# Optimization experiments

Measured on AMD Instinct MI355X. Metric: run time of the kernel, lower is better.

Reference implementation:

```python
import jax, jax.numpy as jnp
import numpy as np
import math

D_MODEL, N_HEADS, D_HEAD = 1024, 16, 64
INIT_RANGE = 0.02
IGNORE = -100000.0


def setup_inputs() -> dict:
    key = jax.random.key(0)
    ks = jax.random.split(key, 5)
    x = jax.random.normal(ks[0], (2, 2048, D_MODEL), dtype=jnp.float32)
    W_Q = INIT_RANGE * jax.random.normal(ks[1], (N_HEADS, D_MODEL, D_HEAD), dtype=jnp.float32)
    W_K = INIT_RANGE * jax.random.normal(ks[2], (N_HEADS, D_MODEL, D_HEAD), dtype=jnp.float32)
    W_V = INIT_RANGE * jax.random.normal(ks[3], (N_HEADS, D_MODEL, D_HEAD), dtype=jnp.float32)
    # W_O is contracted as 'n_heads d_head d_model' in the original einsum
    W_O = INIT_RANGE * jax.random.normal(ks[4], (N_HEADS, D_HEAD, D_MODEL), dtype=jnp.float32)
    b_Q = jnp.zeros((N_HEADS, D_HEAD), dtype=jnp.float32)
    b_K = jnp.zeros((N_HEADS, D_HEAD), dtype=jnp.float32)
    b_V = jnp.zeros((N_HEADS, D_HEAD), dtype=jnp.float32)
    b_O = jnp.zeros((D_MODEL,), dtype=jnp.float32)
    return {"normalized_resid_pre": x, "W_Q": W_Q, "b_Q": b_Q, "W_K": W_K, "b_K": b_K,
            "W_V": W_V, "b_V": b_V, "W_O": W_O, "b_O": b_O}


def reference(normalized_resid_pre, W_Q, b_Q, W_K, b_K, W_V, b_V, W_O, b_O):
    x = normalized_resid_pre  # [b, s, d_model]
    q = jnp.einsum('bsd,hde->bshe', x, W_Q) + b_Q  # [b, s, h, d_head]
    k = jnp.einsum('bsd,hde->bshe', x, W_K) + b_K
    v = jnp.einsum('bsd,hde->bshe', x, W_V) + b_V
    scores = jnp.einsum('bqhe,bkhe->bhqk', q, k) / math.sqrt(D_HEAD)
    S = x.shape[1]
    causal = jnp.tril(jnp.ones((S, S), dtype=bool))  # True where allowed
    scores = jnp.where(causal, scores, IGNORE)
    pattern = jax.nn.softmax(scores, axis=-1)  # [b, h, q, k]
    z = jnp.einsum('bhqk,bkhe->bqhe', pattern, v)
    attn_out = jnp.einsum('bqhe,hed->bqd', z, W_O) + b_O
    return attn_out
```

## Files before the change

### kernel.cpp

```cpp
#include <hip/hip_runtime.h>
#include <cstdint>
#include <cstddef>

typedef unsigned short u16;
typedef __bf16 bf16x8 __attribute__((ext_vector_type(8)));
typedef _Float16 f16x4 __attribute__((ext_vector_type(4)));
typedef _Float16 f16x2 __attribute__((ext_vector_type(2)));
typedef float  f32x4  __attribute__((ext_vector_type(4)));
typedef unsigned short u16x8 __attribute__((ext_vector_type(8)));
typedef unsigned short u16x4 __attribute__((ext_vector_type(4)));

#define DM   1024
#define NH   16
#define DH   64
#define SS   2048
#define BSZ  4096
#define NQKV 3072
#define QSCALE 0.18033688011f

__device__ __forceinline__ u16 f2b(float f) {
  unsigned u = __builtin_bit_cast(unsigned, f);
  return (u16)((u + 0x7FFFu + ((u >> 16) & 1u)) >> 16);
}
__device__ __forceinline__ u16 f2h(float f) {
  _Float16 h = (_Float16)f;
  return __builtin_bit_cast(u16, h);
}

__device__ __forceinline__ void gl_lds16(const void* g, void* l) {
  __builtin_amdgcn_global_load_lds(
      (__attribute__((address_space(1))) void*)(void*)g,
      (__attribute__((address_space(3))) void*)l, 16, 0, 0);
}

__global__ __launch_bounds__(256) void prep_all_kernel(
    const float* __restrict__ x, u16* __restrict__ xb,
    const float* __restrict__ Wq, const float* __restrict__ Wk,
    const float* __restrict__ Wv, u16* __restrict__ wqkvt,
    const float* __restrict__ Wo, u16* __restrict__ wot) {
  __shared__ __align__(16) u16 Ts[64 * 72];
  int bid = blockIdx.x, t = threadIdx.x;
  if (bid < 2048) {
    int i = (bid * 256 + t) * 8;
    float4 a = *(const float4*)(x + i);
    float4 b = *(const float4*)(x + i + 4);
    u16x8 o;
    o[0] = f2b(a.x); o[1] = f2b(a.y); o[2] = f2b(a.z); o[3] = f2b(a.w);
    o[4] = f2b(b.x); o[5] = f2b(b.y); o[6] = f2b(b.z); o[7] = f2b(b.w);
    *(u16x8*)(xb + i) = o;
    return;
  }
  if (bid < 2816) {
    int idx = bid - 2048;
    int dt = idx & 15, sl = idx >> 4;
    int proj = sl >> 4, h = sl & 15;
    const float* W = (proj == 0) ? Wq : ((proj == 1) ? Wk : Wv);
    int d0 = dt * 64;
    {
      int ld = t >> 2;
      int ec = (t & 3) * 16;
      const float* src = W + ((size_t)h * DM + d0 + ld) * DH + ec;
      float4 v0 = *(const float4*)(src);
      float4 v1 = *(const float4*)(src + 4);
      float4 v2 = *(const float4*)(src + 8);
      float4 v3 = *(const float4*)(src + 12);
      float vv[16] = {v0.x, v0.y, v0.z, v0.w, v1.x, v1.y, v1.z, v1.w,
                      v2.x, v2.y, v2.z, v2.w, v3.x, v3.y, v3.z, v3.w};
#pragma unroll
      for (int i = 0; i < 16; i++) Ts[(ec + i) * 72 + ld] = f2b(vv[i]);
    }
    __syncthreads();
    {
      int le = t >> 2;
      int dc = (t & 3) * 16;
      int n = proj * DM + h * DH + le;
      u16* dst = wqkvt + (size_t)n * DM + d0 + dc;
      *(u16x8*)(dst)     = *(const u16x8*)&Ts[le * 72 + dc];
      *(u16x8*)(dst + 8) = *(const u16x8*)&Ts[le * 72 + dc + 8];
    }
    return;
  }
  {
    int idx = bid - 2816;
    int dt = idx & 15, h = idx >> 4;
    int d0 = dt * 64;
    {
      int le = t >> 2;
      int dc = (t & 3) * 16;
      const float* src = Wo + ((size_t)h * DH + le) * DM + d0 + dc;
      float4 v0 = *(const float4*)(src);
      float4 v1 = *(const float4*)(src + 4);
      float4 v2 = *(const float4*)(src + 8);
      float4 v3 = *(const float4*)(src + 12);
      float vv[16] = {v0.x, v0.y, v0.z, v0.w, v1.x, v1.y, v1.z, v1.w,
                      v2.x, v2.y, v2.z, v2.w, v3.x, v3.y, v3.z, v3.w};
#pragma unroll
      for (int i = 0; i < 16; i++) Ts[(dc + i) * 72 + le] = f2b(vv[i]);
    }
    __syncthreads();
    {
      int ld = t >> 2;
      int ec = (t & 3) * 16;
      u16* dst = wot + (size_t)(d0 + ld) * DM + h * DH + ec;
      *(u16x8*)(dst)     = *(const u16x8*)&Ts[ld * 72 + ec];
      *(u16x8*)(dst + 8) = *(const u16x8*)&Ts[ld * 72 + ec + 8];
    }
  }
}

__global__ __launch_bounds__(256) void gemm_qkv_kernel(
    const u16* __restrict__ A, const u16* __restrict__ Bt,
    u16* __restrict__ o_q, u16* __restrict__ o_k, u16* __restrict__ o_v,
    const float* __restrict__ c0, const float* __restrict__ c1,
    const float* __restrict__ c2) {
  const int K = DM;
  __shared__ __align__(16) u16 As[128 * 32];
  __shared__ __align__(16) u16 Bs[128 * 32];
  __shared__ __align__(16) u16 Cs[64 * 128];
  int t = threadIdx.x, w = t >> 6, l = t & 63;
  int lr = l & 15, lq = l >> 4;
  int m0 = blockIdx.x * 128, n0 = blockIdx.y * 128;
  int wr = w >> 1, wc = w & 1;
  f32x4 acc[4][4] = {};
  const u16* ga = A + (size_t)(m0 + (t >> 2)) * K + (t & 3) * 8;
  const u16* gb = Bt + (size_t)(n0 + (t >> 2)) * K + (t & 3) * 8;

  for (int k0 = 0; k0 < K; k0 += 32) {
    __syncthreads();
    gl_lds16(ga + k0,           &As[w * 512]);
    gl_lds16(ga + k0 + 64 * K,  &As[2048 + w * 512]);
    gl_lds16(gb + k0,           &Bs[w * 512]);
    gl_lds16(gb + k0 + 64 * K,  &Bs[2048 + w * 512]);
    __syncthreads();
    bf16x8 af[4], bfr[4];
#pragma unroll
    for (int i = 0; i < 4; i++)
      af[i] = *(const bf16x8*)&As[(wr * 64 + i * 16 + lr) * 32 + lq * 8];
#pragma unroll
    for (int j = 0; j < 4; j++)
      bfr[j] = *(const bf16x8*)&Bs[(wc * 64 + j * 16 + lr) * 32 + lq * 8];
#pragma unroll
    for (int i = 0; i < 4; i++)
#pragma unroll
      for (int j = 0; j < 4; j++)
        acc[i][j] = __builtin_amdgcn_mfma_f32_16x16x32_bf16(af[i], bfr[j], acc[i][j], 0, 0, 0);
  }

  int proj = n0 >> 10;
  int r0 = n0 & 1023;
  int h0 = r0 >> 6;
  const float* bp = (proj == 0) ? c0 : ((proj == 1) ? c1 : c2);

#pragma unroll
  for (int p = 0; p < 2; p++) {
    __syncthreads();
    if (wr == p) {
#pragma unroll
      for (int j = 0; j < 4; j++) {
        int nl = wc * 64 + j * 16 + lr;
        float bias = bp[r0 + nl];
#pragma unroll
        for (int i = 0; i < 4; i++) {
#pragma unroll
          for (int g = 0; g < 4; g++) {
            int ml = i * 16 + lq * 4 + g;
            float val = acc[i][j][g] + bias;
            if (proj == 0)      Cs[ml * 128 + nl] = f2b(val * QSCALE);
            else if (proj == 1) Cs[ml * 128 + nl] = f2b(val);
            else                Cs[nl * 64 + ml] = f2h(val);
          }
        }
      }
    }
    __syncthreads();
    int m_base = m0 + p * 64;
    if (proj < 2) {
      int ml = t >> 2, q4 = t & 3;
      int hh = q4 >> 1, e0 = (q4 & 1) * 32;
      int m = m_base + ml, b = m >> 11, s = m & 2047;
      int h = h0 + hh;
      u16* dst = (proj == 0 ? o_q : o_k) + ((size_t)(b * NH + h) * SS + s) * DH + e0;
      const u16* src = &Cs[ml * 128 + hh * 64 + e0];
      *(u16x8*)(dst)      = *(const u16x8*)(src);
      *(u16x8*)(dst + 8)  = *(const u16x8*)(src + 8);
      *(u16x8*)(dst + 16) = *(const u16x8*)(src + 16);
      *(u16x8*)(dst + 24) = *(const u16x8*)(src + 24);
    } else {
      int er = t >> 1, sh = t & 1;
      int hh = er >> 6, e = er & 63;
      int h = h0 + hh;
      int ms = m_base + sh * 32, b = ms >> 11, s = ms & 2047;
      u16* dst = o_v + ((size_t)(b * NH + h) * DH + e) * SS + s;
      const u16* src = &Cs[er * 64 + sh * 32];
      *(u16x8*)(dst)      = *(const u16x8*)(src);
      *(u16x8*)(dst + 8)  = *(const u16x8*)(src + 8);
      *(u16x8*)(dst + 16) = *(const u16x8*)(src + 16);
      *(u16x8*)(dst + 24) = *(const u16x8*)(src + 24);
    }
  }
}

__global__ __launch_bounds__(256) void gemm_o_kernel(
    const u16* __restrict__ A, const u16* __restrict__ Bt,
    const float* __restrict__ bo, float* __restrict__ fout) {
  const int K = DM;
  __shared__ __align__(16) u16 As[128 * 32];
  __shared__ __align__(16) u16 Bs[64 * 32];
  int t = threadIdx.x, w = t >> 6, l = t & 63;
  int lr = l & 15, lq = l >> 4;
  int m0 = blockIdx.x * 128, n0 = blockIdx.y * 64;
  f32x4 acc[2][4] = {};
  const u16* ga = A + (size_t)(m0 + (t >> 2)) * K + (t & 3) * 8;
  const u16* gb = Bt + (size_t)(n0 + (t >> 2)) * K + (t & 3) * 8;

  for (int k0 = 0; k0 < K; k0 += 32) {
    __syncthreads();
    gl_lds16(ga + k0,           &As[w * 512]);
    gl_lds16(ga + k0 + 64 * K,  &As[2048 + w * 512]);
    gl_lds16(gb + k0, &Bs[w * 512]);
    __syncthreads();
    bf16x8 af[2], bfr[4];
#pragma unroll
    for (int i = 0; i < 2; i++)
      af[i] = *(const bf16x8*)&As[(w * 32 + i * 16 + lr) * 32 + lq * 8];
#pragma unroll
    for (int j = 0; j < 4; j++)
      bfr[j] = *(const bf16x8*)&Bs[(j * 16 + lr) * 32 + lq * 8];
#pragma unroll
    for (int i = 0; i < 2; i++)
#pragma unroll
      for (int j = 0; j < 4; j++)
        acc[i][j] = __builtin_amdgcn_mfma_f32_16x16x32_bf16(af[i], bfr[j], acc[i][j], 0, 0, 0);
  }

  int mb = m0 + w * 32 + lq * 4;
  int nb = n0 + lr;
#pragma unroll
  for (int j = 0; j < 4; j++) {
    int n = nb + j * 16;
    float bias = bo[n];
#pragma unroll
    for (int i = 0; i < 2; i++) {
#pragma unroll
      for (int g = 0; g < 4; g++) {
        int m = mb + i * 16 + g;
        fout[(size_t)m * DM + n] = acc[i][j][g] + bias;
      }
    }
  }
}

__global__ __launch_bounds__(256) void attn_kernel(const u16* __restrict__ q_ws,
                                                   const u16* __restrict__ k_ws,
                                                   const u16* __restrict__ vt_ws,
                                                   u16* __restrict__ z_ws) {
  __shared__ __align__(16) u16 Ks[2][64 * 72], Vs[2][64 * 72];

  int t = threadIdx.x;
  int w = t >> 6;
  int l = t & 63;
  int lr = l & 15, lq = l >> 4;
  int srow = t >> 3;
  int sc8 = (t & 7) * 8;

  int bid = blockIdx.x;
  int xcd = bid & 7, idx = bid >> 3;
  int bh = xcd * 4 + (idx & 3);
  int p = idx >> 2;
  int bq = p & 7;
  int jt = (p >> 3) ? (15 - bq) : bq;
  const u16* Qb = q_ws + (size_t)bh * SS * DH;
  const u16* Kb = k_ws + (size_t)bh * SS * DH;
  const u16* Vb = vt_ws + (size_t)bh * DH * SS;
  int b = bh >> 4, h16 = bh & 15;

  int q0 = jt * 128;
  int nkt = 2 * jt + 2;
  int my_last = nkt - 2 + (w >> 1);

  int qr0 = q0 + w * 32 + lr;
  bf16x8 qf00 = *(const bf16x8*)(Qb + (size_t)qr0 * DH + lq * 8);
  bf16x8 qf01 = *(const bf16x8*)(Qb + (size_t)qr0 * DH + 32 + lq * 8);
  bf16x8 qf10 = *(const bf16x8*)(Qb + (size_t)(qr0 + 16) * DH + lq * 8);
  bf16x8 qf11 = *(const bf16x8*)(Qb + (size_t)(qr0 + 16) * DH + 32 + lq * 8);

  f32x4 accO0[4] = {}, accO1[4] = {};
  float accL0 = 0.f, accL1 = 0.f;

  {
    const u16* kg = Kb + (size_t)srow * DH + sc8;
    const u16* vg = Vb + (size_t)srow * SS + sc8;
    *(u16x8*)&Ks[0][srow * 72 + sc8] = *(const u16x8*)kg;
    *(u16x8*)&Ks[0][(srow + 32) * 72 + sc8] = *(const u16x8*)(kg + 32 * DH);
    *(u16x8*)&Vs[0][srow * 72 + sc8] = *(const u16x8*)vg;
    *(u16x8*)&Vs[0][(srow + 32) * 72 + sc8] = *(const u16x8*)(vg + (size_t)32 * SS);
  }

  for (int it = 0; it < nkt; ++it) {
    __syncthreads();
    int pb = it & 1;
    bool have_next = (it + 1 < nkt);

    u16x8 rk0, rk1, rv0, rv1;
    if (have_next) {
      int k0n = (it + 1) * 64;
      const u16* kg = Kb + (size_t)(k0n + srow) * DH + sc8;
      const u16* vg = Vb + (size_t)srow * SS + k0n + sc8;
      rk0 = *(const u16x8*)kg;
      rk1 = *(const u16x8*)(kg + 32 * DH);
      rv0 = *(const u16x8*)vg;
      rv1 = *(const u16x8*)(vg + (size_t)32 * SS);
    }

    if (it <= my_last) {
      f32x4 sc0[4], sc1[4];
#pragma unroll
      for (int nt = 0; nt < 4; nt++) {
        bf16x8 kf0 = *(const bf16x8*)&Ks[pb][(nt * 16 + lr) * 72 + lq * 8];
        bf16x8 kf1 = *(const bf16x8*)&Ks[pb][(nt * 16 + lr) * 72 + 32 + lq * 8];
        __builtin_amdgcn_s_setprio(1);
        f32x4 a = {0.f, 0.f, 0.f, 0.f};
        a = __builtin_amdgcn_mfma_f32_16x16x32_bf16(kf0, qf00, a, 0, 0, 0);
        a = __builtin_amdgcn_mfma_f32_16x16x32_bf16(kf1, qf01, a, 0, 0, 0);
        sc0[nt] = a;
        f32x4 c = {0.f, 0.f, 0.f, 0.f};
        c = __builtin_amdgcn_mfma_f32_16x16x32_bf16(kf0, qf10, c, 0, 0, 0);
        c = __builtin_amdgcn_mfma_f32_16x16x32_bf16(kf1, qf11, c, 0, 0, 0);
        sc1[nt] = c;
        __builtin_amdgcn_s_setprio(0);
      }

      if (it == my_last) {
        int k0 = it * 64;
#pragma unroll
        for (int nt = 0; nt < 4; nt++) {
#pragma unroll
          for (int gg = 0; gg < 4; gg++) {
            int gk = k0 + nt * 16 + lq * 4 + gg;
            if (gk > qr0) sc0[nt][gg] = -1e30f;
            if (gk > qr0 + 16) sc1[nt][gg] = -1e30f;
          }
        }
      }

      f16x4 pf0[4], pf1[4];
#pragma unroll
      for (int nt = 0; nt < 4; nt++) {
        float a0 = __builtin_amdgcn_exp2f(sc0[nt][0]);
        float a1 = __builtin_amdgcn_exp2f(sc0[nt][1]);
        float a2 = __builtin_amdgcn_exp2f(sc0[nt][2]);
        float a3 = __builtin_amdgcn_exp2f(sc0[nt][3]);
        accL0 += (a0 + a1) + (a2 + a3);
        f16x2 e0 = __builtin_bit_cast(f16x2, __builtin_amdgcn_cvt_pkrtz(a0, a1));
        f16x2 e1 = __builtin_bit_cast(f16x2, __builtin_amdgcn_cvt_pkrtz(a2, a3));
        pf0[nt][0] = e0[0]; pf0[nt][1] = e0[1];
        pf0[nt][2] = e1[0]; pf0[nt][3] = e1[1];
        float c0v = __builtin_amdgcn_exp2f(sc1[nt][0]);
        float c1v = __builtin_amdgcn_exp2f(sc1[nt][1]);
        float c2v = __builtin_amdgcn_exp2f(sc1[nt][2]);
        float c3v = __builtin_amdgcn_exp2f(sc1[nt][3]);
        accL1 += (c0v + c1v) + (c2v + c3v);
        f16x2 e2 = __builtin_bit_cast(f16x2, __builtin_amdgcn_cvt_pkrtz(c0v, c1v));
        f16x2 e3 = __builtin_bit_cast(f16x2, __builtin_amdgcn_cvt_pkrtz(c2v, c3v));
        pf1[nt][0] = e2[0]; pf1[nt][1] = e2[1];
        pf1[nt][2] = e3[0]; pf1[nt][3] = e3[1];
      }

#pragma unroll
      for (int ks = 0; ks < 4; ks++) {
        f16x4 vfr[4];
#pragma unroll
        for (int et = 0; et < 4; et++)
          vfr[et] = *(const f16x4*)&Vs[pb][(et * 16 + lr) * 72 + ks * 16 + lq * 4];
        __builtin_amdgcn_s_setprio(1);
#pragma unroll
        for (int et = 0; et < 4; et++) {
          accO0[et] = __builtin_amdgcn_mfma_f32_16x16x16f16(vfr[et], pf0[ks], accO0[et], 0, 0, 0);
          accO1[et] = __builtin_amdgcn_mfma_f32_16x16x16f16(vfr[et], pf1[ks], accO1[et], 0, 0, 0);
        }
        __builtin_amdgcn_s_setprio(0);
      }
    }

    if (have_next) {
      int nb = (it + 1) & 1;
      *(u16x8*)&Ks[nb][srow * 72 + sc8] = rk0;
      *(u16x8*)&Ks[nb][(srow + 32) * 72 + sc8] = rk1;
      *(u16x8*)&Vs[nb][srow * 72 + sc8] = rv0;
      *(u16x8*)&Vs[nb][(srow + 32) * 72 + sc8] = rv1;
    }
  }

  accL0 += __shfl_xor(accL0, 16, 64);
  accL0 += __shfl_xor(accL0, 32, 64);
  accL1 += __shfl_xor(accL1, 16, 64);
  accL1 += __shfl_xor(accL1, 32, 64);
  float inv0 = 1.0f / accL0;
  float inv1 = 1.0f / accL1;

  u16* zrow0 = z_ws + ((size_t)(b * SS + qr0)) * DM + h16 * DH;
  u16* zrow1 = z_ws + ((size_t)(b * SS + qr0 + 16)) * DM + h16 * DH;
#pragma unroll
  for (int et = 0; et < 4; et++) {
    u16x4 o0, o1;
#pragma unroll
    for (int gg = 0; gg < 4; gg++) {
      o0[gg] = f2b(accO0[et][gg] * inv0);
      o1[gg] = f2b(accO1[et][gg] * inv1);
    }
    *(u16x4*)(zrow0 + et * 16 + lq * 4) = o0;
    *(u16x4*)(zrow1 + et * 16 + lq * 4) = o1;
  }
}

extern "C" void kernel_launch(void* const* d_in, const int* in_sizes, int n_in,
                              void* d_out, int out_size, void* d_ws, size_t ws_size,
                              hipStream_t stream) {
  const float* x  = (const float*)d_in[0];
  const float* Wq = (const float*)d_in[1];
  const float* bq = (const float*)d_in[2];
  const float* Wk = (const float*)d_in[3];
  const float* bk = (const float*)d_in[4];
  const float* Wv = (const float*)d_in[5];
  const float* bv = (const float*)d_in[6];
  const float* Wo = (const float*)d_in[7];
  const float* bo = (const float*)d_in[8];
  float* out = (float*)d_out;

  char* ws = (char*)d_ws;
  const size_t MB = 1u << 20;
  u16* xb    = (u16*)(ws);
  u16* wqkvt = (u16*)(ws + 8 * MB);
  u16* wot   = (u16*)(ws + 14 * MB);
  u16* q_ws  = (u16*)(ws + 16 * MB);
  u16* k_ws  = (u16*)(ws + 24 * MB);
  u16* vt_ws = (u16*)(ws + 32 * MB);
  u16* z_ws  = (u16*)(ws + 40 * MB);

  prep_all_kernel<<<3072, 256, 0, stream>>>(x, xb, Wq, Wk, Wv, wqkvt, Wo, wot);

  gemm_qkv_kernel<<<dim3(BSZ / 128, NQKV / 128), 256, 0, stream>>>(
      xb, wqkvt, q_ws, k_ws, vt_ws, bq, bk, bv);

  attn_kernel<<<512, 256, 0, stream>>>(q_ws, k_ws, vt_ws, z_ws);

  gemm_o_kernel<<<dim3(BSZ / 128, DM / 64), 256, 0, stream>>>(z_ws, wot, bo, out);
}
```

Baseline: 190.1 us.

## Split-K output projection with atomic accumulation over bias-initialized output

The output projection GEMM is split into two K halves across a new grid dimension, and each half accumulates into the output with atomicAdd. The output is pre-filled with the bias by 1024 extra blocks added to the prep kernel. The goal is to double the block count of the small O-projection GEMM (512 to 1024 blocks) for better CU occupancy. The cost is extra atomic traffic, a full extra output-sized write, and a non-deterministic summation order.

```diff
diff --git a/kernel.cpp b/kernel.cpp
--- a/kernel.cpp
+++ b/kernel.cpp
@@ -37,7 +37,8 @@
     const float* __restrict__ x, u16* __restrict__ xb,
     const float* __restrict__ Wq, const float* __restrict__ Wk,
     const float* __restrict__ Wv, u16* __restrict__ wqkvt,
-    const float* __restrict__ Wo, u16* __restrict__ wot) {
+    const float* __restrict__ Wo, u16* __restrict__ wot,
+    const float* __restrict__ bo, float* __restrict__ out_init) {
   __shared__ __align__(16) u16 Ts[64 * 72];
   int bid = blockIdx.x, t = threadIdx.x;
   if (bid < 2048) {
@@ -80,7 +81,7 @@
     }
     return;
   }
-  {
+  if (bid < 3072) {
     int idx = bid - 2816;
     int dt = idx & 15, h = idx >> 4;
     int d0 = dt * 64;
@@ -105,6 +106,20 @@
       *(u16x8*)(dst)     = *(const u16x8*)&Ts[ld * 72 + ec];
       *(u16x8*)(dst + 8) = *(const u16x8*)&Ts[ld * 72 + ec + 8];
     }
+    return;
+  }
+  {
+    int m = (bid - 3072) * 4 + (t >> 6);
+    int n0 = (t & 63) * 16;
+    float4 b0 = *(const float4*)(bo + n0);
+    float4 b1 = *(const float4*)(bo + n0 + 4);
+    float4 b2 = *(const float4*)(bo + n0 + 8);
+    float4 b3 = *(const float4*)(bo + n0 + 12);
+    float* dst = out_init + (size_t)m * DM + n0;
+    *(float4*)(dst)      = b0;
+    *(float4*)(dst + 4)  = b1;
+    *(float4*)(dst + 8)  = b2;
+    *(float4*)(dst + 12) = b3;
   }
 }
 
@@ -202,18 +217,19 @@
 
 __global__ __launch_bounds__(256) void gemm_o_kernel(
     const u16* __restrict__ A, const u16* __restrict__ Bt,
-    const float* __restrict__ bo, float* __restrict__ fout) {
+    float* __restrict__ fout) {
   const int K = DM;
   __shared__ __align__(16) u16 As[128 * 32];
   __shared__ __align__(16) u16 Bs[64 * 32];
   int t = threadIdx.x, w = t >> 6, l = t & 63;
   int lr = l & 15, lq = l >> 4;
   int m0 = blockIdx.x * 128, n0 = blockIdx.y * 64;
+  int kb = blockIdx.z * 512;
   f32x4 acc[2][4] = {};
   const u16* ga = A + (size_t)(m0 + (t >> 2)) * K + (t & 3) * 8;
   const u16* gb = Bt + (size_t)(n0 + (t >> 2)) * K + (t & 3) * 8;
 
-  for (int k0 = 0; k0 < K; k0 += 32) {
+  for (int k0 = kb; k0 < kb + 512; k0 += 32) {
     __syncthreads();
     gl_lds16(ga + k0,           &As[w * 512]);
     gl_lds16(ga + k0 + 64 * K,  &As[2048 + w * 512]);
@@ -238,13 +254,12 @@
 #pragma unroll
   for (int j = 0; j < 4; j++) {
     int n = nb + j * 16;
-    float bias = bo[n];
 #pragma unroll
     for (int i = 0; i < 2; i++) {
 #pragma unroll
       for (int g = 0; g < 4; g++) {
         int m = mb + i * 16 + g;
-        fout[(size_t)m * DM + n] = acc[i][j][g] + bias;
+        atomicAdd(&fout[(size_t)m * DM + n], acc[i][j][g]);
       }
     }
   }
@@ -437,12 +452,13 @@
   u16* vt_ws = (u16*)(ws + 32 * MB);
   u16* z_ws  = (u16*)(ws + 40 * MB);
 
-  prep_all_kernel<<<3072, 256, 0, stream>>>(x, xb, Wq, Wk, Wv, wqkvt, Wo, wot);
+  prep_all_kernel<<<4096, 256, 0, stream>>>(x, xb, Wq, Wk, Wv, wqkvt, Wo, wot,
+                                            bo, out);
 
   gemm_qkv_kernel<<<dim3(BSZ / 128, NQKV / 128), 256, 0, stream>>>(
       xb, wqkvt, q_ws, k_ws, vt_ws, bq, bk, bv);
 
   attn_kernel<<<512, 256, 0, stream>>>(q_ws, k_ws, vt_ws, z_ws);
 
-  gemm_o_kernel<<<dim3(BSZ / 128, DM / 64), 256, 0, stream>>>(z_ws, wot, bo, out);
-}
+  gemm_o_kernel<<<dim3(BSZ / 128, DM / 64, 2), 256, 0, stream>>>(z_ws, wot, out);
+}
```

Measured after the change: 213.5 us. +12.3%, slower.
